# Performance work log

Measured on AMD Instinct MI355X. Metric: run time of the kernel, lower is better.

Reference implementation:

```python
import jax, jax.numpy as jnp
import numpy as np
import math

EPS = 1e-5

def layernorm(x, w, b):
    mu = jnp.mean(x, axis=-1, keepdims=True)
    var = jnp.mean((x - mu) ** 2, axis=-1, keepdims=True)
    return (x - mu) / jnp.sqrt(var + EPS) * w + b

def pos_encoding(L, D):
    pos = jnp.arange(L, dtype=jnp.float32)[:, None]
    div = jnp.exp(jnp.arange(0, D, 2, dtype=jnp.float32) * (-math.log(10000.0) / D))
    pe = jnp.zeros((L, D), dtype=jnp.float32)
    pe = pe.at[:, 0::2].set(jnp.sin(pos * div))
    pe = pe.at[:, 1::2].set(jnp.cos(pos * div))
    return pe

def ssm_block(x, nw, nb, A, iw, ib, ow, ob):
    # x: [B,L,D]
    z = layernorm(x, nw, nb)
    proj = jnp.einsum('bld,ed->ble', z, iw) + ib  # [B,L,2D]
    u, g = jnp.split(proj, 2, axis=-1)
    g = jax.nn.sigmoid(g)
    u_t = jnp.swapaxes(u, 0, 1)  # [L,B,D]
    g_t = jnp.swapaxes(g, 0, 1)
    h0 = jnp.zeros(x.shape[::2], dtype=x.dtype)  # [B,D]
    def step(h, ug):
        ut, gt = ug
        h = gt * h + (1.0 - gt) * jnp.tanh(A * h + ut)
        return h, h
    _, hs = jax.lax.scan(step, h0, (u_t, g_t))  # hs: [L,B,D]
    out = jnp.einsum('lbd,ed->ble', hs, ow).swapaxes(0, 1).swapaxes(0, 1)
    out = jnp.einsum('lbd,ed->ble', hs, ow) + ob
    return x + out

def mha(x, qkv_w, qkv_b, ao_w, ao_b, nhead):
    B, L, D = x.shape
    dh = D // nhead
    qkv = jnp.einsum('bld,ed->ble', x, qkv_w) + qkv_b  # [B,L,3D]
    q, k, v = jnp.split(qkv, 3, axis=-1)
    def heads(t):
        return t.reshape(B, L, nhead, dh).transpose(0, 2, 1, 3)  # [B,H,L,dh]
    q, k, v = heads(q), heads(k), heads(v)
    scores = jnp.einsum('bhqd,bhkd->bhqk', q, k) / jnp.sqrt(jnp.asarray(dh, x.dtype))
    attn = jax.nn.softmax(scores, axis=-1)
    out = jnp.einsum('bhqk,bhkd->bhqd', attn, v)
    out = out.transpose(0, 2, 1, 3).reshape(B, L, D)
    return jnp.einsum('bld,ed->ble', out, ao_w) + ao_b

def encoder_layer(x, l1w, l1b, l2w, l2b, qkv_w, qkv_b, ao_w, ao_b, f1w, f1b, f2w, f2b, nhead):
    # norm_first pre-LN encoder layer, relu FFN, no dropout (eval)
    x = x + mha(layernorm(x, l1w, l1b), qkv_w, qkv_b, ao_w, ao_b, nhead)
    h = layernorm(x, l2w, l2b)
    h = jax.nn.relu(jnp.einsum('bld,fd->blf', h, f1w) + f1b)
    h = jnp.einsum('blf,df->bld', h, f2w) + f2b
    return x + h

def setup_inputs() -> dict:
    key = jax.random.key(0)
    ks = jax.random.split(key, 16)
    B, L, F, D, S, T = 8, 2048, 64, 128, 2, 2
    s = 0.05
    inp = {
        'x': jax.random.normal(ks[0], (B, L, F), jnp.float32),
        'in_w': jax.random.normal(ks[1], (D, F), jnp.float32) * s,
        'in_b': jnp.zeros((D,), jnp.float32),
        'ssm_norm_w': jnp.ones((S, D), jnp.float32),
        'ssm_norm_b': jnp.zeros((S, D), jnp.float32),
        'ssm_A': jax.random.normal(ks[2], (S, D), jnp.float32) * 0.1,
        'ssm_in_w': jax.random.normal(ks[3], (S, 2 * D, D), jnp.float32) * s,
        'ssm_in_b': jnp.zeros((S, 2 * D), jnp.float32),
        'ssm_out_w': jax.random.normal(ks[4], (S, D, D), jnp.float32) * s,
        'ssm_out_b': jnp.zeros((S, D), jnp.float32),
        'ln1_w': jnp.ones((T, D), jnp.float32),
        'ln1_b': jnp.zeros((T, D), jnp.float32),
        'ln2_w': jnp.ones((T, D), jnp.float32),
        'ln2_b': jnp.zeros((T, D), jnp.float32),
        'qkv_w': jax.random.normal(ks[5], (T, 3 * D, D), jnp.float32) * s,
        'qkv_b': jnp.zeros((T, 3 * D), jnp.float32),
        'ao_w': jax.random.normal(ks[6], (T, D, D), jnp.float32) * s,
        'ao_b': jnp.zeros((T, D), jnp.float32),
        'ff1_w': jax.random.normal(ks[7], (T, 4 * D, D), jnp.float32) * s,
        'ff1_b': jnp.zeros((T, 4 * D), jnp.float32),
        'ff2_w': jax.random.normal(ks[8], (T, D, 4 * D), jnp.float32) * s,
        'ff2_b': jnp.zeros((T, D), jnp.float32),
        'hln_w': jnp.ones((D,), jnp.float32),
        'hln_b': jnp.zeros((D,), jnp.float32),
        'h1_w': jax.random.normal(ks[9], (D, D), jnp.float32) * s,
        'h1_b': jnp.zeros((D,), jnp.float32),
        'h2_w': jax.random.normal(ks[10], (1, D), jnp.float32) * s,
        'h2_b': jnp.zeros((1,), jnp.float32),
    }
    return inp

NHEAD = 4

def reference(x, in_w, in_b, ssm_norm_w, ssm_norm_b, ssm_A, ssm_in_w, ssm_in_b,
              ssm_out_w, ssm_out_b, ln1_w, ln1_b, ln2_w, ln2_b, qkv_w, qkv_b,
              ao_w, ao_b, ff1_w, ff1_b, ff2_w, ff2_b, hln_w, hln_b, h1_w, h1_b,
              h2_w, h2_b):
    B, L, _ = x.shape
    D = in_w.shape[0]
    h = jnp.einsum('blf,df->bld', x, in_w) + in_b
    h = h + pos_encoding(L, D)[None]
    for i in range(ssm_A.shape[0]):
        h = ssm_block(h, ssm_norm_w[i], ssm_norm_b[i], ssm_A[i],
                      ssm_in_w[i], ssm_in_b[i], ssm_out_w[i], ssm_out_b[i])
    for i in range(ln1_w.shape[0]):
        h = encoder_layer(h, ln1_w[i], ln1_b[i], ln2_w[i], ln2_b[i],
                          qkv_w[i], qkv_b[i], ao_w[i], ao_b[i],
                          ff1_w[i], ff1_b[i], ff2_w[i], ff2_b[i], NHEAD)
    pooled = 0.5 * h[:, -1, :] + 0.5 * jnp.mean(h, axis=1)  # [B,D]
    p = layernorm(pooled, hln_w, hln_b)
    p = jax.nn.gelu(p @ h1_w.T + h1_b, approximate=False)
    return p @ h2_w.T + h2_b  # [B,1]
```

## Files before the change

kernel.cpp:

```cpp
#include <hip/hip_runtime.h>
#include <hip/hip_bf16.h>
#include <math.h>

#define L_SEQ 2048
#define D_MODEL 128
#define N_ROWS 16384
#define LOG2E 1.4426950408889634f

typedef __attribute__((ext_vector_type(8))) short bf16x8;
typedef __attribute__((ext_vector_type(4))) short short4v;
typedef __attribute__((ext_vector_type(4))) float f32x4;

__device__ __forceinline__ short f2bf(float x)
{
    __hip_bfloat16 b = __float2bfloat16(x);
    return *reinterpret_cast<short*>(&b);
}
__device__ __forceinline__ short f2bf_fast(float x)
{
    unsigned u = __builtin_bit_cast(unsigned, x);
    return (short)((u + 0x8000u) >> 16);
}
__device__ __forceinline__ unsigned cvt_pk_bf16(float lo, float hi)
{
    unsigned r;
    asm("v_cvt_pk_bf16_f32 %0, %1, %2" : "=v"(r) : "v"(lo), "v"(hi));
    return r;
}
__device__ __forceinline__ float bf2f(short s)
{
    unsigned u = ((unsigned)(unsigned short)s) << 16;
    return __builtin_bit_cast(float, u);
}
__device__ __forceinline__ short f2h(float x)
{
    _Float16 h = (_Float16)x;
    return (short)__builtin_bit_cast(unsigned short, h);
}
__device__ __forceinline__ float h2f(short s)
{
    _Float16 h = __builtin_bit_cast(_Float16, (unsigned short)s);
    return (float)h;
}

__global__ __launch_bounds__(256) void convert_kernel(
    const float* __restrict__ x,    const float* __restrict__ inw,
    const float* __restrict__ ssmi, const float* __restrict__ ssmo,
    const float* __restrict__ qkvw, const float* __restrict__ aow,
    const float* __restrict__ f1w,  const float* __restrict__ f2w,
    short* __restrict__ xb, short* __restrict__ wb)
{
    int it = blockIdx.x * 256 + threadIdx.x;
    const float* src; short* dst; int off;
    if      (it < 131072) { src = x;    dst = xb;          off = it; }
    else if (it < 132096) { src = inw;  dst = wb;          off = it - 131072; }
    else if (it < 140288) { src = ssmi; dst = wb + 8192;   off = it - 132096; }
    else if (it < 144384) { src = ssmo; dst = wb + 73728;  off = it - 140288; }
    else if (it < 156672) { src = qkvw; dst = wb + 106496; off = it - 144384; }
    else if (it < 160768) { src = aow;  dst = wb + 204800; off = it - 156672; }
    else if (it < 177152) { src = f1w;  dst = wb + 237568; off = it - 160768; }
    else                  { src = f2w;  dst = wb + 368640; off = it - 177152; }
    off <<= 3;
    float4 v0 = *(const float4*)(src + off);
    float4 v1 = *(const float4*)(src + off + 4);
    bf16x8 p = {f2bf(v0.x), f2bf(v0.y), f2bf(v0.z), f2bf(v0.w),
                f2bf(v1.x), f2bf(v1.y), f2bf(v1.z), f2bf(v1.w)};
    *(bf16x8*)(dst + off) = p;
}

template <int FUSE>
__global__ __launch_bounds__(256) void gemm_ln(const short* __restrict__ A,
                                               const short* __restrict__ W,
                                               const float* __restrict__ bias,
                                               const float* __restrict__ lnw,
                                               const float* __restrict__ lnb,
                                               float* __restrict__ bh,
                                               short* __restrict__ lnout,
                                               int K)
{
    __shared__ __align__(16) short As[32][72];
    __shared__ __align__(16) short Bs[128][72];
    __shared__ float2 red[2][32];

    const int tid  = threadIdx.x;
    const int wave = tid >> 6;
    const int lane = tid & 63;
    const int m    = lane & 15;
    const int quad = lane >> 4;
    const int rh   = wave & 1;
    const int ch   = wave >> 1;
    const int n0   = blockIdx.x * 32;

    const int arow = tid >> 3, acol = (tid & 7) << 3;
    const int brow = tid >> 1, bcol = (tid & 1) << 5;

    const short* Ap = A + (size_t)(n0 + arow) * K + acol;
    const short* Wp = W + (size_t)brow * K + bcol;

    f32x4 acc[4];
#pragma unroll
    for (int i = 0; i < 4; ++i) acc[i] = (f32x4){0.f, 0.f, 0.f, 0.f};

    bf16x8 a0 = *(const bf16x8*)Ap;
    bf16x8 b0 = *(const bf16x8*)Wp;
    bf16x8 b1 = *(const bf16x8*)(Wp + 8);
    bf16x8 b2 = *(const bf16x8*)(Wp + 16);
    bf16x8 b3 = *(const bf16x8*)(Wp + 24);

    for (int k0 = 0; k0 < K; k0 += 64) {
        *(bf16x8*)&As[arow][acol]      = a0;
        *(bf16x8*)&Bs[brow][bcol]      = b0;
        *(bf16x8*)&Bs[brow][bcol + 8]  = b1;
        *(bf16x8*)&Bs[brow][bcol + 16] = b2;
        *(bf16x8*)&Bs[brow][bcol + 24] = b3;
        __syncthreads();
        if (k0 + 64 < K) {
            a0 = *(const bf16x8*)(Ap + k0 + 64);
            b0 = *(const bf16x8*)(Wp + k0 + 64);
            b1 = *(const bf16x8*)(Wp + k0 + 72);
            b2 = *(const bf16x8*)(Wp + k0 + 80);
            b3 = *(const bf16x8*)(Wp + k0 + 88);
        }
#pragma unroll
        for (int ks = 0; ks < 2; ++ks) {
            bf16x8 af = *(const bf16x8*)&As[(rh << 4) + m][(ks << 5) + (quad << 3)];
#pragma unroll
            for (int nt = 0; nt < 4; ++nt) {
                bf16x8 bfr = *(const bf16x8*)&Bs[(ch << 6) + (nt << 4) + m][(ks << 5) + (quad << 3)];
                acc[nt] = __builtin_amdgcn_mfma_f32_16x16x32_bf16(af, bfr, acc[nt], 0, 0, 0);
            }
        }
        __syncthreads();
    }

#pragma unroll
    for (int nt = 0; nt < 4; ++nt) {
        int col = (ch << 6) + (nt << 4) + m;
        float bv = bias[col];
        float fr = 0.f;
        if (FUSE == 0)
            fr = __expf((float)(col & ~1) * (-0.07195578415606394f));
#pragma unroll
        for (int r = 0; r < 4; ++r) {
            int row = n0 + (rh << 4) + (quad << 2) + r;
            float t = acc[nt][r] + bv;
            if (FUSE == 0) {
                float ang = (float)(row & (L_SEQ - 1)) * fr;
                t += (col & 1) ? cosf(ang) : sinf(ang);
            } else {
                t += bh[(size_t)row * 128 + col];
            }
            acc[nt][r] = t;
            bh[(size_t)row * 128 + col] = t;
        }
    }

    if (FUSE < 2) {
        float wv[4], bvn[4];
#pragma unroll
        for (int nt = 0; nt < 4; ++nt) {
            wv[nt]  = lnw[(ch << 6) + (nt << 4) + m];
            bvn[nt] = lnb[(ch << 6) + (nt << 4) + m];
        }
        float s1[4], s2[4];
#pragma unroll
        for (int r = 0; r < 4; ++r) {
            float s = 0.f, q = 0.f;
#pragma unroll
            for (int nt = 0; nt < 4; ++nt) {
                float t = acc[nt][r];
                s += t;
                q = fmaf(t, t, q);
            }
            s += __shfl_xor(s, 1);  q += __shfl_xor(q, 1);
            s += __shfl_xor(s, 2);  q += __shfl_xor(q, 2);
            s += __shfl_xor(s, 4);  q += __shfl_xor(q, 4);
            s += __shfl_xor(s, 8);  q += __shfl_xor(q, 8);
            s1[r] = s; s2[r] = q;
            if (m == 0) red[ch][(rh << 4) + (quad << 2) + r] = make_float2(s, q);
        }
        __syncthreads();
#pragma unroll
        for (int r = 0; r < 4; ++r) {
            float2 o = red[ch ^ 1][(rh << 4) + (quad << 2) + r];
            float ts = s1[r] + o.x;
            float tq = s2[r] + o.y;
            float mean = ts * (1.f / 128.f);
            float var  = tq * (1.f / 128.f) - mean * mean;
            float inv  = rsqrtf(var + 1e-5f);
            int row = n0 + (rh << 4) + (quad << 2) + r;
#pragma unroll
            for (int nt = 0; nt < 4; ++nt) {
                int col = (ch << 6) + (nt << 4) + m;
                lnout[(size_t)row * 128 + col] =
                    f2bf((acc[nt][r] - mean) * inv * wv[nt] + bvn[nt]);
            }
        }
    }
}

enum { EPI_BF_RELU = 0, EPI_QKV = 1, EPI_SCAN_T = 2 };

template <int EPI>
__global__ __launch_bounds__(256) void gemm_bf(const short* __restrict__ A,
                                               const short* __restrict__ W,
                                               const float* __restrict__ bias,
                                               short* __restrict__ outb,
                                               short* __restrict__ outv,
                                               int K, int E)
{
    __shared__ __align__(16) short As[64][136];
    __shared__ __align__(16) short Bs[64][136];

    const int tid  = threadIdx.x;
    const int wave = tid >> 6;
    const int lane = tid & 63;
    const int m    = lane & 15;
    const int quad = lane >> 4;

    const int n0 = blockIdx.y * 64;
    const int e0 = blockIdx.x * 64;

    const int srow = tid >> 2;
    const int scol = (tid & 3) << 5;

    const short* Ap = A + (size_t)(n0 + srow) * K + scol;
    const short* Wp = W + (size_t)(e0 + srow) * K + scol;

    bf16x8 a0 = *(const bf16x8*)(Ap);
    bf16x8 a1 = *(const bf16x8*)(Ap + 8);
    bf16x8 a2 = *(const bf16x8*)(Ap + 16);
    bf16x8 a3 = *(const bf16x8*)(Ap + 24);
    bf16x8 w0 = *(const bf16x8*)(Wp);
    bf16x8 w1 = *(const bf16x8*)(Wp + 8);
    bf16x8 w2 = *(const bf16x8*)(Wp + 16);
    bf16x8 w3 = *(const bf16x8*)(Wp + 24);
    *(bf16x8*)&As[srow][scol]      = a0;
    *(bf16x8*)&As[srow][scol + 8]  = a1;
    *(bf16x8*)&As[srow][scol + 16] = a2;
    *(bf16x8*)&As[srow][scol + 24] = a3;
    *(bf16x8*)&Bs[srow][scol]      = w0;
    *(bf16x8*)&Bs[srow][scol + 8]  = w1;
    *(bf16x8*)&Bs[srow][scol + 16] = w2;
    *(bf16x8*)&Bs[srow][scol + 24] = w3;
    __syncthreads();

    f32x4 acc[4];
#pragma unroll
    for (int i = 0; i < 4; ++i) acc[i] = (f32x4){0.f, 0.f, 0.f, 0.f};

#pragma unroll
    for (int ks = 0; ks < 4; ++ks) {
        bf16x8 af = *(const bf16x8*)&As[(wave << 4) + m][(ks << 5) + (quad << 3)];
#pragma unroll
        for (int nt = 0; nt < 4; ++nt) {
            bf16x8 bfr = *(const bf16x8*)&Bs[(nt << 4) + m][(ks << 5) + (quad << 3)];
            acc[nt] = __builtin_amdgcn_mfma_f32_16x16x32_bf16(af, bfr, acc[nt], 0, 0, 0);
        }
    }

    if (EPI == EPI_QKV) {
        const float QSC = 0.17677669529663687f * LOG2E;
        if (e0 < 256) {
            short* dst = (e0 < 128) ? outb : (outb + 2097152);
            int cbase = (e0 < 128) ? e0 : (e0 - 128);
#pragma unroll
            for (int nt = 0; nt < 4; ++nt) {
                int col = cbase + (nt << 4) + m;
                float bv = bias[e0 + (nt << 4) + m];
#pragma unroll
                for (int r = 0; r < 4; ++r) {
                    int row = n0 + (wave << 4) + (quad << 2) + r;
                    float v = acc[nt][r] + bv;
                    if (e0 < 128) v *= QSC;
                    dst[(size_t)row * 128 + col] = f2bf(v);
                }
            }
        } else {
            int bb_ = n0 >> 11;
            int l0  = (n0 & (L_SEQ - 1)) + (wave << 4) + (quad << 2);
#pragma unroll
            for (int nt = 0; nt < 4; ++nt) {
                int c  = (e0 - 256) + (nt << 4) + m;
                int hh = c >> 5, dd = c & 31;
                float bv = bias[e0 + (nt << 4) + m];
                short4v pk;
#pragma unroll
                for (int r = 0; r < 4; ++r) pk[r] = f2bf(acc[nt][r] + bv);
                *(short4v*)&outv[(size_t)((bb_ * 4 + hh) * 32 + dd) * L_SEQ + l0] = pk;
            }
        }
    } else if (EPI == EPI_SCAN_T) {
        int bb_ = n0 >> 11;
        int l0  = (n0 & (L_SEQ - 1)) + (wave << 4) + (quad << 2);
#pragma unroll
        for (int nt = 0; nt < 4; ++nt) {
            int col = e0 + (nt << 4) + m;
            float bv = bias[col];
            short4v pk;
            if (e0 < 128) {
#pragma unroll
                for (int r = 0; r < 4; ++r)
                    pk[r] = f2h((acc[nt][r] + bv) * (2.f * LOG2E));
            } else {
#pragma unroll
                for (int r = 0; r < 4; ++r) {
                    float gr = acc[nt][r] + bv;
                    float g = __builtin_amdgcn_rcpf(
                        1.f + __builtin_amdgcn_exp2f(-gr * LOG2E));
                    pk[r] = f2h(g);
                }
            }
            *(short4v*)&outb[(((size_t)(bb_ * 256 + col)) << 11) + l0] = pk;
        }
    } else {
#pragma unroll
        for (int nt = 0; nt < 4; ++nt) {
            int col = e0 + (nt << 4) + m;
            float bv = bias[col];
#pragma unroll
            for (int r = 0; r < 4; ++r) {
                int row = n0 + (wave << 4) + (quad << 2) + r;
                float v = fmaxf(acc[nt][r] + bv, 0.f);
                outb[(size_t)row * E + col] = f2bf(v);
            }
        }
    }
}

#define SCAN_WARM 128

__device__ __forceinline__ void scan8(float& h, bf16x8 u8, bf16x8 g8,
                                      float a2, short* __restrict__ ob, int l0)
{
#pragma unroll
    for (int i = 0; i < 8; ++i) {
        float u2 = h2f(u8[i]);
        float g  = h2f(g8[i]);
        float omg = 1.f - g;
        float m2  = -2.f * omg;
        float c0 = fmaf(g, h, omg);
        float e2 = __builtin_amdgcn_exp2f(fmaf(a2, h, u2));
        float r  = __builtin_amdgcn_rcpf(1.f + e2);
        h = fmaf(m2, r, c0);
        ob[(l0 + i) * D_MODEL] = f2bf(h);
    }
}

__device__ __forceinline__ void scan8_ns(float& h, bf16x8 u8, bf16x8 g8,
                                         float a2)
{
#pragma unroll
    for (int i = 0; i < 8; ++i) {
        float u2 = h2f(u8[i]);
        float g  = h2f(g8[i]);
        float omg = 1.f - g;
        float m2  = -2.f * omg;
        float c0 = fmaf(g, h, omg);
        float e2 = __builtin_amdgcn_exp2f(fmaf(a2, h, u2));
        float r  = __builtin_amdgcn_rcpf(1.f + e2);
        h = fmaf(m2, r, c0);
    }
}

__global__ __launch_bounds__(64) void scan_kernel(const short* __restrict__ pt,
                                                  const float* __restrict__ A,
                                                  short* __restrict__ hs)
{
    int blk = blockIdx.x;
    int c   = blk & 15;
    int bd  = blk >> 4;
    int b   = bd >> 1;
    int d   = ((bd & 1) << 6) + threadIdx.x;
    float a2 = 2.f * A[d] * LOG2E;
    const short* up = pt + (((size_t)(b * 256 + d)) << 11);
    const short* gp = up + (((size_t)128) << 11);
    short* ob = hs + ((size_t)(b << 11)) * D_MODEL + d;

    const int lw = c << 7;
    float h = 0.f;

    bf16x8 uA0, uA1, gA0, gA1;

    if (c > 0) {
        int l0 = lw - SCAN_WARM;
        uA0 = *(const bf16x8*)(up + l0);
        uA1 = *(const bf16x8*)(up + l0 + 8);
        gA0 = *(const bf16x8*)(gp + l0);
        gA1 = *(const bf16x8*)(gp + l0 + 8);
        for (int l = l0; l < lw; l += 32) {
            bf16x8 uB0 = *(const bf16x8*)(up + l + 16);
            bf16x8 uB1 = *(const bf16x8*)(up + l + 24);
            bf16x8 gB0 = *(const bf16x8*)(gp + l + 16);
            bf16x8 gB1 = *(const bf16x8*)(gp + l + 24);
            scan8_ns(h, uA0, gA0, a2);
            scan8_ns(h, uA1, gA1, a2);
            uA0 = *(const bf16x8*)(up + l + 32);
            uA1 = *(const bf16x8*)(up + l + 40);
            gA0 = *(const bf16x8*)(gp + l + 32);
            gA1 = *(const bf16x8*)(gp + l + 40);
            scan8_ns(h, uB0, gB0, a2);
            scan8_ns(h, uB1, gB1, a2);
        }
    } else {
        uA0 = *(const bf16x8*)(up);
        uA1 = *(const bf16x8*)(up + 8);
        gA0 = *(const bf16x8*)(gp);
        gA1 = *(const bf16x8*)(gp + 8);
    }

    for (int l = lw; l < lw + 128; l += 32) {
        bf16x8 uB0 = *(const bf16x8*)(up + l + 16);
        bf16x8 uB1 = *(const bf16x8*)(up + l + 24);
        bf16x8 gB0 = *(const bf16x8*)(gp + l + 16);
        bf16x8 gB1 = *(const bf16x8*)(gp + l + 24);
        scan8(h, uA0, gA0, a2, ob, l);
        scan8(h, uA1, gA1, a2, ob, l + 8);
        if (l + 32 < lw + 128) {
            uA0 = *(const bf16x8*)(up + l + 32);
            uA1 = *(const bf16x8*)(up + l + 40);
            gA0 = *(const bf16x8*)(gp + l + 32);
            gA1 = *(const bf16x8*)(gp + l + 40);
        }
        scan8(h, uB0, gB0, a2, ob, l + 16);
        scan8(h, uB1, gB1, a2, ob, l + 24);
    }
}

__global__ __launch_bounds__(256) void attn_kernel(const short* __restrict__ Qs,
                                                   const short* __restrict__ Ks,
                                                   const short* __restrict__ Vtg,
                                                   short* __restrict__ outb)
{
    __shared__ __align__(16) short Klds[2][64][40];
    __shared__ __align__(16) short Vlds[2][32][72];
    __shared__ __align__(16) short Plds[4][32][68];

    const int tid  = threadIdx.x;
    const int wave = tid >> 6;
    const int lane = tid & 63;
    const int m    = lane & 15;
    const int quad = lane >> 4;

    const int raw = blockIdx.x;
    const int bid = (raw & 7) * 64 + (raw >> 3);
    const int b  = bid >> 6;
    const int h  = (bid >> 4) & 3;
    const int q0 = (bid & 15) << 7;

    const size_t qrow = (size_t)((b << 11) + q0 + (wave << 5) + m);
    bf16x8 qfA = *(const bf16x8*)&Qs[qrow * 128 + (h << 5) + (quad << 3)];
    bf16x8 qfB = *(const bf16x8*)&Qs[(qrow + 16) * 128 + (h << 5) + (quad << 3)];

    f32x4 O00 = {0.f,0.f,0.f,0.f}, O01 = {0.f,0.f,0.f,0.f};
    f32x4 O10 = {0.f,0.f,0.f,0.f}, O11 = {0.f,0.f,0.f,0.f};
    float rs0 = 0.f, rs1 = 0.f;

    const int krow = tid >> 2, dg = (tid & 3) << 3;
    const int vrow = tid >> 3, kg = (tid & 7) << 3;
    const short* kbase = Ks + ((size_t)(b << 11) + krow) * 128 + (h << 5) + dg;
    const short* vbase = Vtg + ((size_t)((b << 2) + h) * 32 + vrow) * L_SEQ + kg;

    bf16x8 kreg = *(const bf16x8*)kbase;
    bf16x8 vreg = *(const bf16x8*)vbase;
    *(bf16x8*)&Klds[0][krow][dg] = kreg;
    *(bf16x8*)&Vlds[0][vrow][kg] = vreg;
    __syncthreads();

    for (int kc = 0; kc < 32; ++kc) {
        const int cur = kc & 1;
        if (kc < 31) {
            kreg = *(const bf16x8*)(kbase + (size_t)((kc + 1) << 6) * 128);
            vreg = *(const bf16x8*)(vbase + ((kc + 1) << 6));
        }

#pragma unroll
        for (int kt = 0; kt < 4; ++kt) {
            bf16x8 kf = *(const bf16x8*)&Klds[cur][(kt << 4) + m][quad << 3];
            f32x4 S0 = __builtin_amdgcn_mfma_f32_16x16x32_bf16(
                kf, qfA, (f32x4){0.f, 0.f, 0.f, 0.f}, 0, 0, 0);
            f32x4 S1 = __builtin_amdgcn_mfma_f32_16x16x32_bf16(
                kf, qfB, (f32x4){0.f, 0.f, 0.f, 0.f}, 0, 0, 0);
            float a0 = __builtin_amdgcn_exp2f(S0[0]);
            float a1 = __builtin_amdgcn_exp2f(S0[1]);
            float a2 = __builtin_amdgcn_exp2f(S0[2]);
            float a3 = __builtin_amdgcn_exp2f(S0[3]);
            rs0 += a0 + a1 + a2 + a3;
            uint2 pkA;
            pkA.x = cvt_pk_bf16(a0, a1);
            pkA.y = cvt_pk_bf16(a2, a3);
            *(uint2*)&Plds[wave][m][(kt << 4) + (quad << 2)] = pkA;
            float b0 = __builtin_amdgcn_exp2f(S1[0]);
            float b1 = __builtin_amdgcn_exp2f(S1[1]);
            float b2 = __builtin_amdgcn_exp2f(S1[2]);
            float b3 = __builtin_amdgcn_exp2f(S1[3]);
            rs1 += b0 + b1 + b2 + b3;
            uint2 pkB;
            pkB.x = cvt_pk_bf16(b0, b1);
            pkB.y = cvt_pk_bf16(b2, b3);
            *(uint2*)&Plds[wave][16 + m][(kt << 4) + (quad << 2)] = pkB;
        }

#pragma unroll
        for (int kt2 = 0; kt2 < 2; ++kt2) {
            short4v aLo = *(const short4v*)&Plds[wave][m][(kt2 << 5) + (quad << 3)];
            short4v aHi = *(const short4v*)&Plds[wave][m][(kt2 << 5) + (quad << 3) + 4];
            bf16x8 pfA = {aLo[0], aLo[1], aLo[2], aLo[3],
                          aHi[0], aHi[1], aHi[2], aHi[3]};
            short4v bLo = *(const short4v*)&Plds[wave][16 + m][(kt2 << 5) + (quad << 3)];
            short4v bHi = *(const short4v*)&Plds[wave][16 + m][(kt2 << 5) + (quad << 3) + 4];
            bf16x8 pfB = {bLo[0], bLo[1], bLo[2], bLo[3],
                          bHi[0], bHi[1], bHi[2], bHi[3]};
            bf16x8 vf0 = *(const bf16x8*)&Vlds[cur][m][(kt2 << 5) + (quad << 3)];
            bf16x8 vf1 = *(const bf16x8*)&Vlds[cur][16 + m][(kt2 << 5) + (quad << 3)];
            O00 = __builtin_amdgcn_mfma_f32_16x16x32_bf16(pfA, vf0, O00, 0, 0, 0);
            O01 = __builtin_amdgcn_mfma_f32_16x16x32_bf16(pfA, vf1, O01, 0, 0, 0);
            O10 = __builtin_amdgcn_mfma_f32_16x16x32_bf16(pfB, vf0, O10, 0, 0, 0);
            O11 = __builtin_amdgcn_mfma_f32_16x16x32_bf16(pfB, vf1, O11, 0, 0, 0);
        }

        if (kc < 31) {
            *(bf16x8*)&Klds[cur ^ 1][krow][dg] = kreg;
            *(bf16x8*)&Vlds[cur ^ 1][vrow][kg] = vreg;
        }
        __syncthreads();
    }

    rs0 += __shfl_xor(rs0, 16);
    rs0 += __shfl_xor(rs0, 32);
    rs1 += __shfl_xor(rs1, 16);
    rs1 += __shfl_xor(rs1, 32);

#pragma unroll
    for (int r = 0; r < 4; ++r) {
        float svA = __shfl(rs0, (quad << 2) + r);
        float svB = __shfl(rs1, (quad << 2) + r);
        float invA = 1.f / svA;
        float invB = 1.f / svB;
        int rowA = (b << 11) + q0 + (wave << 5) + (quad << 2) + r;
        short* opA = outb + (size_t)rowA * D_MODEL + (h << 5) + m;
        opA[0]  = f2bf(O00[r] * invA);
        opA[16] = f2bf(O01[r] * invA);
        short* opB = opA + (size_t)16 * D_MODEL;
        opB[0]  = f2bf(O10[r] * invB);
        opB[16] = f2bf(O11[r] * invB);
    }
}

__global__ __launch_bounds__(1024) void pool_head_kernel(
    const float* __restrict__ h,
    const float* __restrict__ hlnw, const float* __restrict__ hlnb,
    const float* __restrict__ h1w, const float* __restrict__ h1b,
    const float* __restrict__ h2w, const float* __restrict__ h2b,
    float* __restrict__ out)
{
    __shared__ float part[8][128];
    __shared__ float sd[128];
    __shared__ float sq[128];

    int b   = blockIdx.x;
    int t   = threadIdx.x;
    int d   = t & 127;
    int seg = t >> 7;
    const float* hb = h + (size_t)b * L_SEQ * D_MODEL;

    float acc = 0.f;
    int l0 = seg << 8;
    for (int l = l0; l < l0 + 256; l += 4) {
        acc += hb[(l + 0) * D_MODEL + d] + hb[(l + 1) * D_MODEL + d]
             + hb[(l + 2) * D_MODEL + d] + hb[(l + 3) * D_MODEL + d];
    }
    part[seg][d] = acc;
    __syncthreads();

    float v = 0.f;
    if (t < 128) {
        float s = 0.f;
#pragma unroll
        for (int i = 0; i < 8; ++i) s += part[i][t];
        v = 0.5f * hb[(L_SEQ - 1) * D_MODEL + t] + 0.5f * (s * (1.f / (float)L_SEQ));
        sd[t] = v;
    }
    __syncthreads();
    for (int s = 64; s > 0; s >>= 1) {
        if (t < s) sd[t] += sd[t + s];
        __syncthreads();
    }
    float mu = sd[0] * (1.f / 128.f);
    __syncthreads();
    float dv = v - mu;
    if (t < 128) sd[t] = dv * dv;
    __syncthreads();
    for (int s = 64; s > 0; s >>= 1) {
        if (t < s) sd[t] += sd[t + s];
        __syncthreads();
    }
    float var = sd[0] * (1.f / 128.f);
    __syncthreads();
    if (t < 128) sq[t] = dv * rsqrtf(var + 1e-5f) * hlnw[t] + hlnb[t];
    __syncthreads();
    if (t < 128) {
        float dot = h1b[t];
        for (int d2 = 0; d2 < 128; ++d2) dot = fmaf(sq[d2], h1w[t * 128 + d2], dot);
        float ge = 0.5f * dot * (1.f + erff(dot * 0.7071067811865475f));
        sd[t] = ge * h2w[t];
    }
    __syncthreads();
    for (int s = 64; s > 0; s >>= 1) {
        if (t < s) sd[t] += sd[t + s];
        __syncthreads();
    }
    if (t == 0) out[b] = sd[0] + h2b[0];
}

extern "C" void kernel_launch(void* const* d_in, const int* in_sizes, int n_in,
                              void* d_out, int out_size, void* d_ws, size_t ws_size,
                              hipStream_t stream)
{
    (void)in_sizes; (void)n_in; (void)out_size; (void)ws_size;
    const float* x      = (const float*)d_in[0];
    const float* in_w   = (const float*)d_in[1];
    const float* in_b   = (const float*)d_in[2];
    const float* ssm_nw = (const float*)d_in[3];
    const float* ssm_nb = (const float*)d_in[4];
    const float* ssm_A  = (const float*)d_in[5];
    const float* ssm_iw = (const float*)d_in[6];
    const float* ssm_ib = (const float*)d_in[7];
    const float* ssm_ow = (const float*)d_in[8];
    const float* ssm_ob = (const float*)d_in[9];
    const float* ln1w   = (const float*)d_in[10];
    const float* ln1b   = (const float*)d_in[11];
    const float* ln2w   = (const float*)d_in[12];
    const float* ln2b   = (const float*)d_in[13];
    const float* qkvw   = (const float*)d_in[14];
    const float* qkvb   = (const float*)d_in[15];
    const float* aow    = (const float*)d_in[16];
    const float* aob    = (const float*)d_in[17];
    const float* f1w    = (const float*)d_in[18];
    const float* f1b    = (const float*)d_in[19];
    const float* f2w    = (const float*)d_in[20];
    const float* f2b    = (const float*)d_in[21];
    const float* hlnw   = (const float*)d_in[22];
    const float* hlnb   = (const float*)d_in[23];
    const float* h1w    = (const float*)d_in[24];
    const float* h1b    = (const float*)d_in[25];
    const float* h2w    = (const float*)d_in[26];
    const float* h2b    = (const float*)d_in[27];
    float* out = (float*)d_out;

    char* wsb = (char*)d_ws;
    float* bh     = (float*)(wsb);
    short* abuf   = (short*)(wsb + 8388608);
    short* bbuf   = (short*)(wsb + 25165824);
    short* qs     = (short*)(wsb + 29360128);
    short* vt     = (short*)(wsb + 37748736);
    short* xb     = (short*)(wsb + 41943040);
    short* wb     = (short*)(wsb + 44040192);
    short* ks     = qs + 2097152;

    dim3 blk(256);

    convert_kernel<<<756, blk, 0, stream>>>(x, in_w, ssm_iw, ssm_ow, qkvw, aow, f1w, f2w, xb, wb);

    gemm_ln<0><<<512, blk, 0, stream>>>(
        xb, wb, in_b, ssm_nw, ssm_nb, bh, bbuf, 64);

    gemm_bf<EPI_SCAN_T><<<dim3(4, 256), blk, 0, stream>>>(
        bbuf, wb + 8192, ssm_ib, abuf, nullptr, 128, 256);
    scan_kernel<<<256, 64, 0, stream>>>(abuf, ssm_A, bbuf);
    gemm_ln<1><<<512, blk, 0, stream>>>(
        bbuf, wb + 73728, ssm_ob, ssm_nw + 128, ssm_nb + 128, bh, bbuf, 128);

    gemm_bf<EPI_SCAN_T><<<dim3(4, 256), blk, 0, stream>>>(
        bbuf, wb + 8192 + 32768, ssm_ib + 256, abuf, nullptr, 128, 256);
    scan_kernel<<<256, 64, 0, stream>>>(abuf, ssm_A + 128, bbuf);
    gemm_ln<1><<<512, blk, 0, stream>>>(
        bbuf, wb + 73728 + 16384, ssm_ob + 128, ln1w, ln1b, bh, bbuf, 128);

    gemm_bf<EPI_QKV><<<dim3(6, 256), blk, 0, stream>>>(
        bbuf, wb + 106496, qkvb, qs, vt, 128, 384);
    attn_kernel<<<512, blk, 0, stream>>>(qs, ks, vt, bbuf);
    gemm_ln<1><<<512, blk, 0, stream>>>(
        bbuf, wb + 204800, aob, ln2w, ln2b, bh, bbuf, 128);
    gemm_bf<EPI_BF_RELU><<<dim3(8, 256), blk, 0, stream>>>(
        bbuf, wb + 237568, f1b, abuf, nullptr, 128, 512);
    gemm_ln<1><<<512, blk, 0, stream>>>(
        abuf, wb + 368640, f2b, ln1w + 128, ln1b + 128, bh, bbuf, 512);

    gemm_bf<EPI_QKV><<<dim3(6, 256), blk, 0, stream>>>(
        bbuf, wb + 106496 + 49152, qkvb + 384, qs, vt, 128, 384);
    attn_kernel<<<512, blk, 0, stream>>>(qs, ks, vt, bbuf);
    gemm_ln<1><<<512, blk, 0, stream>>>(
        bbuf, wb + 204800 + 16384, aob + 128, ln2w + 128, ln2b + 128, bh, bbuf, 128);
    gemm_bf<EPI_BF_RELU><<<dim3(8, 256), blk, 0, stream>>>(
        bbuf, wb + 237568 + 65536, f1b + 512, abuf, nullptr, 128, 512);
    gemm_ln<2><<<512, blk, 0, stream>>>(
        abuf, wb + 368640 + 65536, f2b + 128, nullptr, nullptr, bh, nullptr, 512);

    pool_head_kernel<<<8, 1024, 0, stream>>>(bh, hlnw, hlnb, h1w, h1b, h2w, h2b, out);
}
```

Before: 343.1 us.

## Split attention over two KV halves with a separate reduction kernel

The attention kernel now splits each query tile's key/value range into two halves, launching twice as many blocks. Each half writes unnormalized fp32 partial outputs and row sums to workspace, and a new reduce kernel combines them, normalizes, and writes bf16. This raises parallelism, since 512 blocks underfill a 256-CU device. In exchange it adds fp32 partial-output traffic and an extra kernel launch. Combining the halves without a max is valid because the softmax is computed without max subtraction.

```diff
diff --git a/kernel.cpp b/kernel.cpp
--- a/kernel.cpp
+++ b/kernel.cpp
@@ -430,7 +430,8 @@
 __global__ __launch_bounds__(256) void attn_kernel(const short* __restrict__ Qs,
                                                    const short* __restrict__ Ks,
                                                    const short* __restrict__ Vtg,
-                                                   short* __restrict__ outb)
+                                                   float* __restrict__ pO,
+                                                   float* __restrict__ prs)
 {
     __shared__ __align__(16) short Klds[2][64][40];
     __shared__ __align__(16) short Vlds[2][32][72];
@@ -443,10 +444,13 @@
     const int quad = lane >> 4;
 
     const int raw = blockIdx.x;
-    const int bid = (raw & 7) * 64 + (raw >> 3);
-    const int b  = bid >> 6;
-    const int h  = (bid >> 4) & 3;
-    const int q0 = (bid & 15) << 7;
+    const int bid = (raw & 7) * 128 + (raw >> 3);
+    const int b    = bid >> 7;
+    const int h    = (bid >> 5) & 3;
+    const int qh   = bid & 31;
+    const int q0   = (qh >> 1) << 7;
+    const int half = qh & 1;
+    const int kv0  = half << 10;
 
     const size_t qrow = (size_t)((b << 11) + q0 + (wave << 5) + m);
     bf16x8 qfA = *(const bf16x8*)&Qs[qrow * 128 + (h << 5) + (quad << 3)];
@@ -458,8 +462,8 @@
 
     const int krow = tid >> 2, dg = (tid & 3) << 3;
     const int vrow = tid >> 3, kg = (tid & 7) << 3;
-    const short* kbase = Ks + ((size_t)(b << 11) + krow) * 128 + (h << 5) + dg;
-    const short* vbase = Vtg + ((size_t)((b << 2) + h) * 32 + vrow) * L_SEQ + kg;
+    const short* kbase = Ks + ((size_t)((b << 11) + kv0) + krow) * 128 + (h << 5) + dg;
+    const short* vbase = Vtg + ((size_t)((b << 2) + h) * 32 + vrow) * L_SEQ + kv0 + kg;
 
     bf16x8 kreg = *(const bf16x8*)kbase;
     bf16x8 vreg = *(const bf16x8*)vbase;
@@ -467,9 +471,9 @@
     *(bf16x8*)&Vlds[0][vrow][kg] = vreg;
     __syncthreads();
 
-    for (int kc = 0; kc < 32; ++kc) {
+    for (int kc = 0; kc < 16; ++kc) {
         const int cur = kc & 1;
-        if (kc < 31) {
+        if (kc < 15) {
             kreg = *(const bf16x8*)(kbase + (size_t)((kc + 1) << 6) * 128);
             vreg = *(const bf16x8*)(vbase + ((kc + 1) << 6));
         }
@@ -519,7 +523,7 @@
             O11 = __builtin_amdgcn_mfma_f32_16x16x32_bf16(pfB, vf1, O11, 0, 0, 0);
         }
 
-        if (kc < 31) {
+        if (kc < 15) {
             *(bf16x8*)&Klds[cur ^ 1][krow][dg] = kreg;
             *(bf16x8*)&Vlds[cur ^ 1][vrow][kg] = vreg;
         }
@@ -531,20 +535,46 @@
     rs1 += __shfl_xor(rs1, 16);
     rs1 += __shfl_xor(rs1, 32);
 
+    const int rowbase = (b << 11) + q0 + (wave << 5);
+    if (quad == 0) {
+        prs[(size_t)((half << 2) + h) * N_ROWS + rowbase + m]      = rs0;
+        prs[(size_t)((half << 2) + h) * N_ROWS + rowbase + 16 + m] = rs1;
+    }
+
+    float* pb = pO + (size_t)(half * N_ROWS) * 128;
 #pragma unroll
     for (int r = 0; r < 4; ++r) {
-        float svA = __shfl(rs0, (quad << 2) + r);
-        float svB = __shfl(rs1, (quad << 2) + r);
-        float invA = 1.f / svA;
-        float invB = 1.f / svB;
-        int rowA = (b << 11) + q0 + (wave << 5) + (quad << 2) + r;
-        short* opA = outb + (size_t)rowA * D_MODEL + (h << 5) + m;
-        opA[0]  = f2bf(O00[r] * invA);
-        opA[16] = f2bf(O01[r] * invA);
-        short* opB = opA + (size_t)16 * D_MODEL;
-        opB[0]  = f2bf(O10[r] * invB);
-        opB[16] = f2bf(O11[r] * invB);
-    }
+        int rowA = rowbase + (quad << 2) + r;
+        float* opA = pb + (size_t)rowA * 128 + (h << 5) + m;
+        opA[0]  = O00[r];
+        opA[16] = O01[r];
+        float* opB = opA + (size_t)16 * 128;
+        opB[0]  = O10[r];
+        opB[16] = O11[r];
+    }
+}
+
+__global__ __launch_bounds__(256) void attn_reduce(const float* __restrict__ pO,
+                                                   const float* __restrict__ prs,
+                                                   short* __restrict__ outb)
+{
+    int idx = blockIdx.x * 256 + threadIdx.x;
+    int row = idx >> 4;
+    int cg  = (idx & 15) << 3;
+    int h   = cg >> 5;
+    float rs = prs[(size_t)h * N_ROWS + row] + prs[(size_t)(4 + h) * N_ROWS + row];
+    float inv = 1.f / rs;
+    const float* p0 = pO + (size_t)row * 128 + cg;
+    const float* p1 = p0 + (size_t)N_ROWS * 128;
+    float4 a0 = *(const float4*)p0;
+    float4 a1 = *(const float4*)(p0 + 4);
+    float4 b0 = *(const float4*)p1;
+    float4 b1 = *(const float4*)(p1 + 4);
+    bf16x8 o = {f2bf((a0.x + b0.x) * inv), f2bf((a0.y + b0.y) * inv),
+                f2bf((a0.z + b0.z) * inv), f2bf((a0.w + b0.w) * inv),
+                f2bf((a1.x + b1.x) * inv), f2bf((a1.y + b1.y) * inv),
+                f2bf((a1.z + b1.z) * inv), f2bf((a1.w + b1.w) * inv)};
+    *(bf16x8*)&outb[(size_t)row * 128 + cg] = o;
 }
 
 __global__ __launch_bounds__(1024) void pool_head_kernel(
@@ -656,6 +686,8 @@
     short* vt     = (short*)(wsb + 37748736);
     short* xb     = (short*)(wsb + 41943040);
     short* wb     = (short*)(wsb + 44040192);
+    float* pO     = (float*)(wsb + 46137344);
+    float* prs    = (float*)(wsb + 62914560);
     short* ks     = qs + 2097152;
 
     dim3 blk(256);
@@ -679,7 +711,8 @@
 
     gemm_bf<EPI_QKV><<<dim3(6, 256), blk, 0, stream>>>(
         bbuf, wb + 106496, qkvb, qs, vt, 128, 384);
-    attn_kernel<<<512, blk, 0, stream>>>(qs, ks, vt, bbuf);
+    attn_kernel<<<1024, blk, 0, stream>>>(qs, ks, vt, pO, prs);
+    attn_reduce<<<1024, blk, 0, stream>>>(pO, prs, bbuf);
     gemm_ln<1><<<512, blk, 0, stream>>>(
         bbuf, wb + 204800, aob, ln2w, ln2b, bh, bbuf, 128);
     gemm_bf<EPI_BF_RELU><<<dim3(8, 256), blk, 0, stream>>>(
@@ -689,7 +722,8 @@
 
     gemm_bf<EPI_QKV><<<dim3(6, 256), blk, 0, stream>>>(
         bbuf, wb + 106496 + 49152, qkvb + 384, qs, vt, 128, 384);
-    attn_kernel<<<512, blk, 0, stream>>>(qs, ks, vt, bbuf);
+    attn_kernel<<<1024, blk, 0, stream>>>(qs, ks, vt, pO, prs);
+    attn_reduce<<<1024, blk, 0, stream>>>(pO, prs, bbuf);
     gemm_ln<1><<<512, blk, 0, stream>>>(
         bbuf, wb + 204800 + 16384, aob + 128, ln2w + 128, ln2b + 128, bh, bbuf, 128);
     gemm_bf<EPI_BF_RELU><<<dim3(8, 256), blk, 0, stream>>>(
```

Result: no change. 343.1 us (-0.0%).
